# Performance work log

Hardware: AMD Instinct MI355X
Metric: run time of the kernel (lower is better)

Reference implementation:

```python
import jax, jax.numpy as jnp
import numpy as np

H = 256          # decoder_size
MAX_LENGTH = 64
VOCAB = 3


def _cell(x, h, c, w_ih, w_hh, b_ih, b_hh):
    # PyTorch LSTM cell, gate order i, f, g, o
    g = x @ w_ih.T + h @ w_hh.T + b_ih + b_hh
    i, f, gg, o = jnp.split(g, 4, axis=-1)
    c = jax.nn.sigmoid(f) * c + jax.nn.sigmoid(i) * jnp.tanh(gg)
    h = jax.nn.sigmoid(o) * jnp.tanh(c)
    return h, c


def _final_state(xs, w_ih, w_hh, b_ih, b_hh):
    # run a unidirectional LSTM over xs [T,B,D], return final (h, c)
    B = xs.shape[1]
    h0 = jnp.zeros((B, H), xs.dtype)
    c0 = jnp.zeros((B, H), xs.dtype)
    def step(carry, x):
        h, c = _cell(x, carry[0], carry[1], w_ih, w_hh, b_ih, b_hh)
        return (h, c), None
    (h, c), _ = jax.lax.scan(step, (h0, c0), xs)
    return h, c


def setup_inputs() -> dict:
    key = jax.random.key(0)
    ks = jax.random.split(key, 20)
    T, B, D = 512, 128, 1024
    s = jnp.float32(0.05)  # keep gates out of saturation
    def p(k, shape):
        return jax.random.normal(k, shape, jnp.float32) * s
    return {
        "x": jax.random.normal(ks[0], (T, B, D), jnp.float32),
        "ew_ih_f": p(ks[1], (4 * H, D)), "ew_hh_f": p(ks[2], (4 * H, H)),
        "eb_ih_f": p(ks[3], (4 * H,)),   "eb_hh_f": p(ks[4], (4 * H,)),
        "ew_ih_b": p(ks[5], (4 * H, D)), "ew_hh_b": p(ks[6], (4 * H, H)),
        "eb_ih_b": p(ks[7], (4 * H,)),   "eb_hh_b": p(ks[8], (4 * H,)),
        "dw_ih0": p(ks[9], (4 * H, H)),  "dw_hh0": p(ks[10], (4 * H, H)),
        "db_ih0": p(ks[11], (4 * H,)),   "db_hh0": p(ks[12], (4 * H,)),
        "dw_ih1": p(ks[13], (4 * H, H)), "dw_hh1": p(ks[14], (4 * H, H)),
        "db_ih1": p(ks[15], (4 * H,)),   "db_hh1": p(ks[16], (4 * H,)),
        "lw": p(ks[17], (VOCAB, H)),     "lb": p(ks[18], (VOCAB,)),
    }


def reference(x, ew_ih_f, ew_hh_f, eb_ih_f, eb_hh_f,
              ew_ih_b, ew_hh_b, eb_ih_b, eb_hh_b,
              dw_ih0, dw_hh0, db_ih0, db_hh0,
              dw_ih1, dw_hh1, db_ih1, db_hh1,
              lw, lb):
    # --- bidirectional encoder: only final hidden states are used ---
    hf, cf = _final_state(x, ew_ih_f, ew_hh_f, eb_ih_f, eb_hh_f)          # forward dir
    hb, cb = _final_state(x[::-1], ew_ih_b, ew_hh_b, eb_ih_b, eb_hh_b)    # backward dir
    # encoder h_n/c_n stacked as [fwd, bwd] -> decoder layer0, layer1 init
    B = x.shape[1]
    inp0 = jnp.zeros((B, H), x.dtype)
    def step(carry, _):
        inp, h0, c0, h1, c1 = carry
        h0, c0 = _cell(inp, h0, c0, dw_ih0, dw_hh0, db_ih0, db_hh0)
        h1, c1 = _cell(h0, h1, c1, dw_ih1, dw_hh1, db_ih1, db_hh1)
        out = h1 @ lw.T + lb  # [B, VOCAB]
        return (h1, h0, c0, h1, c1), out
    _, outs = jax.lax.scan(step, (inp0, hf, cf, hb, cb), None, length=MAX_LENGTH)
    return outs  # [MAX_LENGTH, B, VOCAB]
```

## Files before the change

kernel.cpp:

```cpp
#include <hip/hip_runtime.h>
#include <hip/hip_bf16.h>
#include <math.h>


typedef unsigned short u16;
typedef unsigned int u32;
typedef unsigned long long u64;
typedef _Float16 f16;
typedef f16 f16x8 __attribute__((ext_vector_type(8)));
typedef u16 u16x8 __attribute__((ext_vector_type(8)));
typedef u32 u32x4 __attribute__((ext_vector_type(4)));
typedef float f32x4 __attribute__((ext_vector_type(4)));

__device__ __forceinline__ u16 f2h(float f) {
  return __builtin_bit_cast(unsigned short, (f16)f);
}
__device__ __forceinline__ float h2f(u16 h) {
  return (float)__builtin_bit_cast(f16, h);
}
__device__ __forceinline__ u32 packf16(float a, float b) {
  return (u32)f2h(a) | ((u32)f2h(b) << 16);
}
__device__ __forceinline__ u64 ald64(const u64* p) {
  return __hip_atomic_load(p, __ATOMIC_RELAXED, __HIP_MEMORY_SCOPE_AGENT);
}
__device__ __forceinline__ void ast64(u64* p, u64 v) {
  __hip_atomic_store(p, v, __ATOMIC_RELAXED, __HIP_MEMORY_SCOPE_AGENT);
}

#define SENT 0xFFFFFFFFFFFFFFFFull

__global__ __launch_bounds__(256) void init_k(u32* hglob, u32* r0, u32* r1) {
  int gid = blockIdx.x * 256 + threadIdx.x;
  if (gid < 131072)       hglob[gid] = 0xFFFFFFFFu;
  else if (gid < 196608)  r0[gid - 131072] = 0xFFFFFFFFu;
  else                    r1[gid - 196608] = 0xFFFFFFFFu;
}

__global__ __launch_bounds__(256) void convert_k(
    const float* __restrict__ x,
    const float* __restrict__ wfm, const float* __restrict__ wbm,
    const float* __restrict__ bif, const float* __restrict__ bhf,
    const float* __restrict__ bib, const float* __restrict__ bhb,
    const float* __restrict__ dbi0, const float* __restrict__ dbh0,
    const float* __restrict__ dbi1, const float* __restrict__ dbh1,
    u16* __restrict__ xh, u16* __restrict__ wh,
    float* __restrict__ bias2, float* __restrict__ dbias) {
  const long NX = 67108864L, NW = 1048576L;
  long gid = (long)blockIdx.x * 256 + threadIdx.x;
  if (gid < 1024) {
    bias2[gid]        = bif[gid] + bhf[gid];
    bias2[1024 + gid] = bib[gid] + bhb[gid];
    dbias[gid]        = dbi0[gid] + dbh0[gid];
    dbias[1024 + gid] = dbi1[gid] + dbh1[gid];
  }
  long total4 = (NX + 2 * NW) >> 2;
  long stride = (long)gridDim.x * 256;
  for (long q = gid; q < total4; q += stride) {
    long i = q << 2;
    const float* src; u16* dst; long o;
    if (i < NX)            { src = x;   dst = xh;      o = i; }
    else if (i < NX + NW)  { src = wfm; dst = wh;      o = i - NX; }
    else                   { src = wbm; dst = wh + NW; o = i - NX - NW; }
    float4 v = *(const float4*)&src[o];
    dst[o + 0] = f2h(v.x); dst[o + 1] = f2h(v.y);
    dst[o + 2] = f2h(v.z); dst[o + 3] = f2h(v.w);
  }
}

__global__ __launch_bounds__(256) void convert_we3_k(
    const float* __restrict__ whf, const float* __restrict__ whb,
    u16* __restrict__ wenc3) {
  int o = blockIdx.x * 256 + threadIdx.x;
  int j = o & 7, lane = (o >> 3) & 63, ks = (o >> 9) & 7;
  int w = (o >> 12) & 3, cg = (o >> 14) & 15, d = o >> 18;
  int ri = lane & 15;
  int gcol = (ri & 3) * 256 + cg * 16 + w * 4 + (ri >> 2);
  int k = ks * 32 + (lane >> 4) * 8 + j;
  const float* wsrc = d ? whb : whf;
  wenc3[o] = f2h(wsrc[gcol * 256 + k]);
}

__global__ __launch_bounds__(256) void convert_wdec_k(
    const float* __restrict__ wi0, const float* __restrict__ wh0,
    const float* __restrict__ wi1, const float* __restrict__ wh1,
    u16* __restrict__ wdec) {
  int o = blockIdx.x * 256 + threadIdx.x;
  int j = o & 7, lane = (o >> 3) & 63, ks = (o >> 9) & 15;
  int w = (o >> 13) & 3, cg = (o >> 15) & 15, L = o >> 19;
  int ri = lane & 15;
  int row = (ri & 3) * 256 + cg * 16 + w * 4 + (ri >> 2);
  int k = ks * 32 + (lane >> 4) * 8 + j;
  const float* wi = L ? wi1 : wi0;
  const float* wh = L ? wh1 : wh0;
  float v = (k < 256) ? wi[row * 256 + k] : wh[row * 256 + k - 256];
  wdec[o] = f2h(v);
}

__global__ __launch_bounds__(256) void xproj_gemm(
    const u16* __restrict__ xh, const u16* __restrict__ wh,
    const float* __restrict__ bias2, float* __restrict__ xp) {
  __shared__ u16 Al[128][40];
  __shared__ u16 Bl[128][40];
  int bid = blockIdx.x;
  int dir = bid >> 12, rem = bid & 4095, tb = rem >> 3, nb = rem & 7;
  int tsrc = dir ? (511 - tb) : tb;
  const u16* A  = xh + (long)tsrc * (128 * 1024);
  const u16* Bw = wh + (long)dir * (1024 * 1024) + (long)nb * (128 * 1024);
  float* C = xp + ((long)(dir * 512 + tb) * 128) * 1024 + nb * 128;
  const float* bias = bias2 + dir * 1024 + nb * 128;

  int tid = threadIdx.x, lane = tid & 63, wid = tid >> 6;
  int wr = wid >> 1, wc = wid & 1;
  int srow = tid >> 1, scol = (tid & 1) * 16;
  int fr = lane & 15, ko = lane >> 4;

  f32x4 acc[4][4] = {};
  for (int k0 = 0; k0 < 1024; k0 += 32) {
    u16x8 a0 = *(const u16x8*)&A[(long)srow * 1024 + k0 + scol];
    u16x8 a1 = *(const u16x8*)&A[(long)srow * 1024 + k0 + scol + 8];
    u16x8 b0 = *(const u16x8*)&Bw[(long)srow * 1024 + k0 + scol];
    u16x8 b1 = *(const u16x8*)&Bw[(long)srow * 1024 + k0 + scol + 8];
    __syncthreads();
    *(u16x8*)&Al[srow][scol]     = a0;
    *(u16x8*)&Al[srow][scol + 8] = a1;
    *(u16x8*)&Bl[srow][scol]     = b0;
    *(u16x8*)&Bl[srow][scol + 8] = b1;
    __syncthreads();
    f16x8 af[4], bf[4];
#pragma unroll
    for (int i = 0; i < 4; ++i)
      af[i] = __builtin_bit_cast(f16x8, *(const u16x8*)&Al[wr * 64 + i * 16 + fr][ko * 8]);
#pragma unroll
    for (int jf = 0; jf < 4; ++jf)
      bf[jf] = __builtin_bit_cast(f16x8, *(const u16x8*)&Bl[wc * 64 + jf * 16 + fr][ko * 8]);
#pragma unroll
    for (int i = 0; i < 4; ++i)
#pragma unroll
      for (int jf = 0; jf < 4; ++jf)
        acc[i][jf] = __builtin_amdgcn_mfma_f32_16x16x32_f16(af[i], bf[jf], acc[i][jf], 0, 0, 0);
  }
  int fq = lane >> 4;
#pragma unroll
  for (int i = 0; i < 4; ++i)
#pragma unroll
    for (int jf = 0; jf < 4; ++jf) {
      int col = wc * 64 + jf * 16 + fr;
      float bv = bias[col];
#pragma unroll
      for (int e = 0; e < 4; ++e) {
        int row = wr * 64 + i * 16 + fq * 4 + e;
        C[(long)row * 1024 + col] = acc[i][jf][e] + bv;
      }
    }
}

__global__ __launch_bounds__(256, 1) void encoder_k(
    const u16* __restrict__ wenc3, const float* __restrict__ xp,
    u32* hglob,
    float* h0b, float* h1b, float* cfb, float* cbb) {
  int b = blockIdx.x;
  int g16 = ((b >> 7) << 3) | (b & 7);
  int cg = (b >> 3) & 15;
  int d = g16 >> 3, bg = g16 & 7;
  int tid = threadIdx.x, lane = tid & 63, w = tid >> 6;
  int brow = lane & 15, lq = lane >> 4;
  int hswz = (brow & 7) << 4;

  __shared__ __align__(16) char hlds[2][8192];
  __shared__ __align__(16) u16 hstage[16][16];

  f16x8 wfr[8];
  {
    const u16* wb = wenc3 + (((long)d * 16 + cg) * 4 + w) * 4096 + lane * 8;
#pragma unroll
    for (int ks = 0; ks < 8; ++ks)
      wfr[ks] = __builtin_bit_cast(f16x8, *(const u16x8*)(wb + (long)ks * 512));
  }

  float c_state = 0.f;
  long xpbase = ((long)(d * 512) * 128 + bg * 16 + brow) * 1024 + cg * 16 + w * 4 + lq;
  float xpv[4], xpn[4];
#pragma unroll
  for (int g = 0; g < 4; ++g) xpv[g] = xp[xpbase + g * 256];

  u64* hg = (u64*)hglob;
  long ringbase = (long)g16 * 4096;
  int gcg = tid >> 4, gbrow = tid & 15;
  int gldsbase = gbrow * 512 + gcg * 32;
  int gswz = (gbrow & 7) << 4;
  __syncthreads();

  for (int t = 0; t < 512; ++t) {
    if (t != 0) {
      const long gb = ringbase + (long)(t & 3) * 1024 + 4 * tid;
      u64 v0 = SENT, v1 = SENT, v2 = SENT, v3 = SENT;
      for (;;) {
        bool ok = true;
        if (v0 == SENT) { v0 = ald64(hg + gb + 0); ok &= (v0 != SENT); }
        if (v1 == SENT) { v1 = ald64(hg + gb + 1); ok &= (v1 != SENT); }
        if (v2 == SENT) { v2 = ald64(hg + gb + 2); ok &= (v2 != SENT); }
        if (v3 == SENT) { v3 = ald64(hg + gb + 3); ok &= (v3 != SENT); }
        if (ok) break;
      }
      if (tid < 64)
        ast64(hg + ringbase + (long)((t + 2) & 3) * 1024 + cg * 64 + tid, SENT);
#pragma unroll
      for (int g = 0; g < 4; ++g) xpv[g] = xpn[g];
      char* hwr = hlds[t & 1];
      *(u32x4*)(hwr + (gldsbase ^ gswz)) =
          (u32x4){ (u32)v0, (u32)(v0 >> 32), (u32)v1, (u32)(v1 >> 32) };
      *(u32x4*)(hwr + ((gldsbase + 16) ^ gswz)) =
          (u32x4){ (u32)v2, (u32)(v2 >> 32), (u32)v3, (u32)(v3 >> 32) };
    }
    if (t < 511) {
      long xb2 = xpbase + (long)(t + 1) * 131072;
#pragma unroll
      for (int g = 0; g < 4; ++g) xpn[g] = xp[xb2 + g * 256];
    }
    __syncthreads();

    f32x4 acc0 = {}, acc1 = {};
    if (t != 0) {
      const char* hrd = hlds[t & 1];
#pragma unroll
      for (int ks = 0; ks < 8; ++ks) {
        f16x8 hf = *(const f16x8*)(hrd + ((brow * 512 + ks * 64 + lq * 16) ^ hswz));
        if (ks & 1) acc1 = __builtin_amdgcn_mfma_f32_16x16x32_f16(wfr[ks], hf, acc1, 0, 0, 0);
        else        acc0 = __builtin_amdgcn_mfma_f32_16x16x32_f16(wfr[ks], hf, acc0, 0, 0, 0);
      }
    }

    float iv = 1.f / (1.f + expf(-(acc0[0] + acc1[0] + xpv[0])));
    float fv = 1.f / (1.f + expf(-(acc0[1] + acc1[1] + xpv[1])));
    float gg = tanhf(acc0[2] + acc1[2] + xpv[2]);
    float ov = 1.f / (1.f + expf(-(acc0[3] + acc1[3] + xpv[3])));
    c_state = fv * c_state + iv * gg;
    float hval = ov * tanhf(c_state);

    if (t < 511) {
      hstage[brow][w * 4 + lq] = f2h(hval);
      __syncthreads();
      asm volatile("s_waitcnt vmcnt(0)" ::: "memory");
      if (tid < 64) {
        u64 v = *(const u64*)&hstage[tid >> 2][(tid & 3) * 4];
        ast64(hg + ringbase + (long)((t + 1) & 3) * 1024 + cg * 64 + tid, v);
      }
    } else {
      int rowg = bg * 16 + brow, colg = cg * 16 + w * 4 + lq;
      (d ? h1b : h0b)[32768 + rowg * 256 + colg] = hval;
      (d ? cbb : cfb)[rowg * 256 + colg] = c_state;
    }
  }
}

__global__ __launch_bounds__(256, 1) void decoder_k(
    const u16* __restrict__ wdec, const float* __restrict__ dbias,
    const float* __restrict__ h0b, const float* __restrict__ h1b,
    const float* __restrict__ cfb, const float* __restrict__ cbb,
    u32* r0, u32* r1, float* __restrict__ hist) {
  int b = blockIdx.x;
  int bg = b & 7, cg = b >> 3;
  int tid = threadIdx.x, lane = tid & 63, w = tid >> 6;
  int brow = lane & 15, lq = lane >> 4;
  int hswz = (brow & 7) << 4;
  int col = cg * 16 + w * 4 + lq;

  __shared__ __align__(16) char hA[8192];
  __shared__ __align__(16) char hB[8192];
  __shared__ __align__(16) u16 hstage[16][16];

  f16x8 w0[16], w1[16];
  {
    const u16* p0 = wdec + ((long)(cg * 4 + w)) * 8192 + lane * 8;
    const u16* p1 = wdec + ((long)((16 + cg) * 4 + w)) * 8192 + lane * 8;
#pragma unroll
    for (int ks = 0; ks < 16; ++ks) {
      w0[ks] = __builtin_bit_cast(f16x8, *(const u16x8*)(p0 + (long)ks * 512));
      w1[ks] = __builtin_bit_cast(f16x8, *(const u16x8*)(p1 + (long)ks * 512));
    }
  }
  float b0[4], b1[4];
#pragma unroll
  for (int g = 0; g < 4; ++g) {
    b0[g] = dbias[g * 256 + col];
    b1[g] = dbias[1024 + g * 256 + col];
  }
  float c0 = cfb[(bg * 16 + brow) * 256 + col];
  float c1 = cbb[(bg * 16 + brow) * 256 + col];

  int gbrow = tid & 15, gcg = tid >> 4;
  int gldsbase = gbrow * 512 + gcg * 32;
  int gswz = (gbrow & 7) << 4;
  {
    const float* sA = h0b + 32768 + (bg * 16 + gbrow) * 256 + gcg * 16;
    const float* sB = h1b + 32768 + (bg * 16 + gbrow) * 256 + gcg * 16;
    u32 wa[8], wb[8];
#pragma unroll
    for (int i = 0; i < 8; ++i) {
      wa[i] = packf16(sA[2 * i], sA[2 * i + 1]);
      wb[i] = packf16(sB[2 * i], sB[2 * i + 1]);
    }
    *(u32x4*)(hA + (gldsbase ^ gswz))        = (u32x4){wa[0], wa[1], wa[2], wa[3]};
    *(u32x4*)(hA + ((gldsbase + 16) ^ gswz)) = (u32x4){wa[4], wa[5], wa[6], wa[7]};
    *(u32x4*)(hB + (gldsbase ^ gswz))        = (u32x4){wb[0], wb[1], wb[2], wb[3]};
    *(u32x4*)(hB + ((gldsbase + 16) ^ gswz)) = (u32x4){wb[4], wb[5], wb[6], wb[7]};
  }
  __syncthreads();

  u64* g0 = (u64*)r0;
  u64* g1 = (u64*)r1;
  long ring = (long)bg * 4096;

  for (int t = 0; t < 64; ++t) {
    f32x4 a0 = {}, a1 = {};
    if (t > 0) {
#pragma unroll
      for (int ks = 0; ks < 8; ++ks) {
        f16x8 hf = *(const f16x8*)(hB + ((brow * 512 + ks * 64 + lq * 16) ^ hswz));
        if (ks & 1) a1 = __builtin_amdgcn_mfma_f32_16x16x32_f16(w0[ks], hf, a1, 0, 0, 0);
        else        a0 = __builtin_amdgcn_mfma_f32_16x16x32_f16(w0[ks], hf, a0, 0, 0, 0);
      }
    }
#pragma unroll
    for (int ks = 0; ks < 8; ++ks) {
      f16x8 hf = *(const f16x8*)(hA + ((brow * 512 + ks * 64 + lq * 16) ^ hswz));
      if (ks & 1) a1 = __builtin_amdgcn_mfma_f32_16x16x32_f16(w0[8 + ks], hf, a1, 0, 0, 0);
      else        a0 = __builtin_amdgcn_mfma_f32_16x16x32_f16(w0[8 + ks], hf, a0, 0, 0, 0);
    }
    {
      float iv = 1.f / (1.f + expf(-(a0[0] + a1[0] + b0[0])));
      float fv = 1.f / (1.f + expf(-(a0[1] + a1[1] + b0[1])));
      float gg = tanhf(a0[2] + a1[2] + b0[2]);
      float ov = 1.f / (1.f + expf(-(a0[3] + a1[3] + b0[3])));
      c0 = fv * c0 + iv * gg;
      float h0v = ov * tanhf(c0);
      hstage[brow][w * 4 + lq] = f2h(h0v);
    }
    __syncthreads();
    if (tid < 64)
      ast64(g0 + ring + (long)((t + 2) & 3) * 1024 + cg * 64 + tid, SENT);
    asm volatile("s_waitcnt vmcnt(0)" ::: "memory");
    if (tid < 64) {
      u64 v = *(const u64*)&hstage[tid >> 2][(tid & 3) * 4];
      ast64(g0 + ring + (long)(t & 3) * 1024 + cg * 64 + tid, v);
    }
    {
      const long gb = ring + (long)(t & 3) * 1024 + 4 * tid;
      u64 v0 = SENT, v1 = SENT, v2 = SENT, v3 = SENT;
      for (;;) {
        bool ok = true;
        if (v0 == SENT) { v0 = ald64(g0 + gb + 0); ok &= (v0 != SENT); }
        if (v1 == SENT) { v1 = ald64(g0 + gb + 1); ok &= (v1 != SENT); }
        if (v2 == SENT) { v2 = ald64(g0 + gb + 2); ok &= (v2 != SENT); }
        if (v3 == SENT) { v3 = ald64(g0 + gb + 3); ok &= (v3 != SENT); }
        if (ok) break;
      }
      *(u32x4*)(hA + (gldsbase ^ gswz)) =
          (u32x4){ (u32)v0, (u32)(v0 >> 32), (u32)v1, (u32)(v1 >> 32) };
      *(u32x4*)(hA + ((gldsbase + 16) ^ gswz)) =
          (u32x4){ (u32)v2, (u32)(v2 >> 32), (u32)v3, (u32)(v3 >> 32) };
    }
    __syncthreads();

    a0 = (f32x4){}; a1 = (f32x4){};
#pragma unroll
    for (int ks = 0; ks < 8; ++ks) {
      f16x8 hf = *(const f16x8*)(hA + ((brow * 512 + ks * 64 + lq * 16) ^ hswz));
      if (ks & 1) a1 = __builtin_amdgcn_mfma_f32_16x16x32_f16(w1[ks], hf, a1, 0, 0, 0);
      else        a0 = __builtin_amdgcn_mfma_f32_16x16x32_f16(w1[ks], hf, a0, 0, 0, 0);
    }
#pragma unroll
    for (int ks = 0; ks < 8; ++ks) {
      f16x8 hf = *(const f16x8*)(hB + ((brow * 512 + ks * 64 + lq * 16) ^ hswz));
      if (ks & 1) a1 = __builtin_amdgcn_mfma_f32_16x16x32_f16(w1[8 + ks], hf, a1, 0, 0, 0);
      else        a0 = __builtin_amdgcn_mfma_f32_16x16x32_f16(w1[8 + ks], hf, a0, 0, 0, 0);
    }
    {
      float iv = 1.f / (1.f + expf(-(a0[0] + a1[0] + b1[0])));
      float fv = 1.f / (1.f + expf(-(a0[1] + a1[1] + b1[1])));
      float gg = tanhf(a0[2] + a1[2] + b1[2]);
      float ov = 1.f / (1.f + expf(-(a0[3] + a1[3] + b1[3])));
      c1 = fv * c1 + iv * gg;
      float h1v = ov * tanhf(c1);
      hstage[brow][w * 4 + lq] = f2h(h1v);
    }
    __syncthreads();
    if (tid < 64) {
      u64 v = *(const u64*)&hstage[tid >> 2][(tid & 3) * 4];
      float4 hv4 = { h2f((u16)v), h2f((u16)(v >> 16)),
                     h2f((u16)(v >> 32)), h2f((u16)(v >> 48)) };
      *(float4*)&hist[((long)t * 128 + bg * 16 + (tid >> 2)) * 256 + cg * 16 + (tid & 3) * 4] = hv4;
    }
    if (t < 63) {
      if (tid < 64)
        ast64(g1 + ring + (long)((t + 2) & 3) * 1024 + cg * 64 + tid, SENT);
      asm volatile("s_waitcnt vmcnt(0)" ::: "memory");
      if (tid < 64) {
        u64 v = *(const u64*)&hstage[tid >> 2][(tid & 3) * 4];
        ast64(g1 + ring + (long)(t & 3) * 1024 + cg * 64 + tid, v);
      }
      const long gb = ring + (long)(t & 3) * 1024 + 4 * tid;
      u64 v0 = SENT, v1 = SENT, v2 = SENT, v3 = SENT;
      for (;;) {
        bool ok = true;
        if (v0 == SENT) { v0 = ald64(g1 + gb + 0); ok &= (v0 != SENT); }
        if (v1 == SENT) { v1 = ald64(g1 + gb + 1); ok &= (v1 != SENT); }
        if (v2 == SENT) { v2 = ald64(g1 + gb + 2); ok &= (v2 != SENT); }
        if (v3 == SENT) { v3 = ald64(g1 + gb + 3); ok &= (v3 != SENT); }
        if (ok) break;
      }
      *(u32x4*)(hB + (gldsbase ^ gswz)) =
          (u32x4){ (u32)v0, (u32)(v0 >> 32), (u32)v1, (u32)(v1 >> 32) };
      *(u32x4*)(hB + ((gldsbase + 16) ^ gswz)) =
          (u32x4){ (u32)v2, (u32)(v2 >> 32), (u32)v3, (u32)(v3 >> 32) };
    }
    __syncthreads();
  }
}

__global__ __launch_bounds__(256) void logits_k(
    const float* __restrict__ hist, const float* __restrict__ lw,
    const float* __restrict__ lb, float* __restrict__ out) {
  int widx = threadIdx.x >> 6, lane = threadIdx.x & 63;
  int row = blockIdx.x * 4 + widx;
  const float* h = hist + (long)row * 256;
  float4 hv = *(const float4*)&h[lane * 4];
  float s[3];
#pragma unroll
  for (int v = 0; v < 3; ++v) {
    float4 wv = *(const float4*)&lw[v * 256 + lane * 4];
    float p = hv.x * wv.x + hv.y * wv.y + hv.z * wv.z + hv.w * wv.w;
#pragma unroll
    for (int o = 32; o > 0; o >>= 1) p += __shfl_xor(p, o, 64);
    s[v] = p;
  }
  if (lane == 0) {
    out[row * 3 + 0] = s[0] + lb[0];
    out[row * 3 + 1] = s[1] + lb[1];
    out[row * 3 + 2] = s[2] + lb[2];
  }
}

extern "C" void kernel_launch(void* const* d_in, const int* in_sizes, int n_in,
                              void* d_out, int out_size, void* d_ws, size_t ws_size,
                              hipStream_t stream) {
  const float* x     = (const float*)d_in[0];
  const float* ewihf = (const float*)d_in[1];
  const float* ewhhf = (const float*)d_in[2];
  const float* ebihf = (const float*)d_in[3];
  const float* ebhhf = (const float*)d_in[4];
  const float* ewihb = (const float*)d_in[5];
  const float* ewhhb = (const float*)d_in[6];
  const float* ebihb = (const float*)d_in[7];
  const float* ebhhb = (const float*)d_in[8];
  const float* dwih0 = (const float*)d_in[9];
  const float* dwhh0 = (const float*)d_in[10];
  const float* dbih0 = (const float*)d_in[11];
  const float* dbhh0 = (const float*)d_in[12];
  const float* dwih1 = (const float*)d_in[13];
  const float* dwhh1 = (const float*)d_in[14];
  const float* dbih1 = (const float*)d_in[15];
  const float* dbhh1 = (const float*)d_in[16];
  const float* lw    = (const float*)d_in[17];
  const float* lb    = (const float*)d_in[18];
  float* out = (float*)d_out;
  (void)in_sizes; (void)n_in; (void)out_size; (void)ws_size;

  char* wsb = (char*)d_ws;
  size_t off = 0;
  auto take = [&](size_t bytes) -> char* {
    char* p = wsb + off;
    off = (off + bytes + 255) & ~(size_t)255;
    return p;
  };
  u16*   xh    = (u16*)take(67108864ull * 2);
  u16*   whx   = (u16*)take(2097152ull * 2);
  float* xp    = (float*)take(134217728ull * 4);
  u16*   wenc3 = (u16*)take(524288ull * 2);
  u16*   wdec  = (u16*)take(1048576ull * 2);
  float* bias2 = (float*)take(2048 * 4);
  float* dbias = (float*)take(2048 * 4);
  u32*   hglob = (u32*)take(131072ull * 4);
  u32*   r0    = (u32*)take(65536ull * 4);
  u32*   r1    = (u32*)take(65536ull * 4);
  float* h0b   = (float*)take(65536 * 4);
  float* h1b   = (float*)take(65536 * 4);
  float* cfb   = (float*)take(32768 * 4);
  float* cbb   = (float*)take(32768 * 4);
  float* hist  = (float*)take(2097152 * 4);

  init_k<<<1024, 256, 0, stream>>>(hglob, r0, r1);
  convert_k<<<2048, 256, 0, stream>>>(x, ewihf, ewihb, ebihf, ebhhf, ebihb, ebhhb,
                                      dbih0, dbhh0, dbih1, dbhh1, xh, whx, bias2, dbias);
  convert_we3_k<<<2048, 256, 0, stream>>>(ewhhf, ewhhb, wenc3);
  convert_wdec_k<<<4096, 256, 0, stream>>>(dwih0, dwhh0, dwih1, dwhh1, wdec);
  xproj_gemm<<<8192, 256, 0, stream>>>(xh, whx, bias2, xp);
  encoder_k<<<256, 256, 0, stream>>>(wenc3, xp, hglob, h0b, h1b, cfb, cbb);
  decoder_k<<<128, 256, 0, stream>>>(wdec, dbias, h0b, h1b, cfb, cbb, r0, r1, hist);
  logits_k<<<2048, 256, 0, stream>>>(hist, lw, lb, out);
}
```

Before: 2.226 ms.

## Repartition encoder recurrence into paired 512-thread blocks with half-hidden ownership

The encoder recurrence moves from 256 blocks (each owning 16 hidden columns and exchanging h through a global ring with all 16 column-group peers) to 32 blocks of 512 threads. Each block owns half the hidden columns for one direction and batch group, keeps 4 weight tiles in registers, and swaps only the other half with a single partner block every step. The aim is to cut cross-block polling and synchronisation latency on the serial 512-step chain. In exchange each block does four times the MFMA and gate work per step, uses far fewer CUs, and raises register pressure.

```diff
diff --git a/kernel.cpp b/kernel.cpp
--- a/kernel.cpp
+++ b/kernel.cpp
@@ -68,17 +68,17 @@
   }
 }
 
-__global__ __launch_bounds__(256) void convert_we3_k(
+__global__ __launch_bounds__(256) void convert_we4_k(
     const float* __restrict__ whf, const float* __restrict__ whb,
-    u16* __restrict__ wenc3) {
+    u16* __restrict__ wenc4) {
   int o = blockIdx.x * 256 + threadIdx.x;
   int j = o & 7, lane = (o >> 3) & 63, ks = (o >> 9) & 7;
-  int w = (o >> 12) & 3, cg = (o >> 14) & 15, d = o >> 18;
+  int tile = (o >> 12) & 3, w = (o >> 14) & 7, half = (o >> 17) & 1, d = o >> 18;
   int ri = lane & 15;
-  int gcol = (ri & 3) * 256 + cg * 16 + w * 4 + (ri >> 2);
+  int gcol = (ri & 3) * 256 + half * 128 + w * 16 + tile * 4 + (ri >> 2);
   int k = ks * 32 + (lane >> 4) * 8 + j;
   const float* wsrc = d ? whb : whf;
-  wenc3[o] = f2h(wsrc[gcol * 256 + k]);
+  wenc4[o] = f2h(wsrc[gcol * 256 + k]);
 }
 
 __global__ __launch_bounds__(256) void convert_wdec_k(
@@ -155,101 +155,101 @@
     }
 }
 
-__global__ __launch_bounds__(256, 1) void encoder_k(
-    const u16* __restrict__ wenc3, const float* __restrict__ xp,
+__global__ __launch_bounds__(512, 2) void encoder_k(
+    const u16* __restrict__ wenc4, const float* __restrict__ xp,
     u32* hglob,
     float* h0b, float* h1b, float* cfb, float* cbb) {
   int b = blockIdx.x;
-  int g16 = ((b >> 7) << 3) | (b & 7);
-  int cg = (b >> 3) & 15;
-  int d = g16 >> 3, bg = g16 & 7;
+  int d = b >> 4, bg = (b >> 1) & 7, half = b & 1;
   int tid = threadIdx.x, lane = tid & 63, w = tid >> 6;
   int brow = lane & 15, lq = lane >> 4;
   int hswz = (brow & 7) << 4;
+  int ohb = half * 256;
+  int phb = (half ^ 1) * 256;
 
   __shared__ __align__(16) char hlds[2][8192];
-  __shared__ __align__(16) u16 hstage[16][16];
-
-  f16x8 wfr[8];
-  {
-    const u16* wb = wenc3 + (((long)d * 16 + cg) * 4 + w) * 4096 + lane * 8;
+  __shared__ __align__(16) u16 hstage[16][128];
+
+  f16x8 wfr[32];
+#pragma unroll
+  for (int tile = 0; tile < 4; ++tile) {
+    const u16* wb = wenc4 + ((((long)(d * 2 + half) * 8 + w) * 4 + tile)) * 4096 + lane * 8;
 #pragma unroll
     for (int ks = 0; ks < 8; ++ks)
-      wfr[ks] = __builtin_bit_cast(f16x8, *(const u16x8*)(wb + (long)ks * 512));
-  }
-
-  float c_state = 0.f;
-  long xpbase = ((long)(d * 512) * 128 + bg * 16 + brow) * 1024 + cg * 16 + w * 4 + lq;
-  float xpv[4], xpn[4];
-#pragma unroll
-  for (int g = 0; g < 4; ++g) xpv[g] = xp[xpbase + g * 256];
+      wfr[tile * 8 + ks] = __builtin_bit_cast(f16x8, *(const u16x8*)(wb + (long)ks * 512));
+  }
+
+  float c_state[4];
+#pragma unroll
+  for (int i = 0; i < 4; ++i) c_state[i] = 0.f;
+
+  long xprow = ((long)(d * 512) * 128 + bg * 16 + brow) * 1024;
+  int xcol0 = half * 128 + w * 16 + lq;
+  float xpv[4][4];
+#pragma unroll
+  for (int tile = 0; tile < 4; ++tile)
+#pragma unroll
+    for (int g = 0; g < 4; ++g)
+      xpv[tile][g] = xp[xprow + g * 256 + xcol0 + tile * 4];
 
   u64* hg = (u64*)hglob;
-  long ringbase = (long)g16 * 4096;
-  int gcg = tid >> 4, gbrow = tid & 15;
-  int gldsbase = gbrow * 512 + gcg * 32;
-  int gswz = (gbrow & 7) << 4;
+  long orbase = (long)(((d * 8 + bg) * 2) + half) * 2048;
+  long prbase = (long)(((d * 8 + bg) * 2) + (half ^ 1)) * 2048;
+  int srow2 = tid >> 5, scolq = tid & 31;
   __syncthreads();
 
   for (int t = 0; t < 512; ++t) {
     if (t != 0) {
-      const long gb = ringbase + (long)(t & 3) * 1024 + 4 * tid;
-      u64 v0 = SENT, v1 = SENT, v2 = SENT, v3 = SENT;
-      for (;;) {
-        bool ok = true;
-        if (v0 == SENT) { v0 = ald64(hg + gb + 0); ok &= (v0 != SENT); }
-        if (v1 == SENT) { v1 = ald64(hg + gb + 1); ok &= (v1 != SENT); }
-        if (v2 == SENT) { v2 = ald64(hg + gb + 2); ok &= (v2 != SENT); }
-        if (v3 == SENT) { v3 = ald64(hg + gb + 3); ok &= (v3 != SENT); }
-        if (ok) break;
-      }
-      if (tid < 64)
-        ast64(hg + ringbase + (long)((t + 2) & 3) * 1024 + cg * 64 + tid, SENT);
-#pragma unroll
-      for (int g = 0; g < 4; ++g) xpv[g] = xpn[g];
-      char* hwr = hlds[t & 1];
-      *(u32x4*)(hwr + (gldsbase ^ gswz)) =
-          (u32x4){ (u32)v0, (u32)(v0 >> 32), (u32)v1, (u32)(v1 >> 32) };
-      *(u32x4*)(hwr + ((gldsbase + 16) ^ gswz)) =
-          (u32x4){ (u32)v2, (u32)(v2 >> 32), (u32)v3, (u32)(v3 >> 32) };
-    }
-    if (t < 511) {
-      long xb2 = xpbase + (long)(t + 1) * 131072;
-#pragma unroll
-      for (int g = 0; g < 4; ++g) xpn[g] = xp[xb2 + g * 256];
-    }
-    __syncthreads();
-
-    f32x4 acc0 = {}, acc1 = {};
+      const u64* pp = hg + prbase + (long)(t & 3) * 512 + tid;
+      u64 v = ald64(pp);
+      while (v == SENT) v = ald64(pp);
+      ast64(hg + orbase + (long)((t + 2) & 3) * 512 + tid, SENT);
+      *(u64*)(hlds[t & 1] + ((srow2 * 512 + phb + scolq * 8) ^ ((srow2 & 7) << 4))) = v;
+    }
+    __syncthreads();
+
+    f32x4 acc[4] = {};
     if (t != 0) {
       const char* hrd = hlds[t & 1];
 #pragma unroll
       for (int ks = 0; ks < 8; ++ks) {
         f16x8 hf = *(const f16x8*)(hrd + ((brow * 512 + ks * 64 + lq * 16) ^ hswz));
-        if (ks & 1) acc1 = __builtin_amdgcn_mfma_f32_16x16x32_f16(wfr[ks], hf, acc1, 0, 0, 0);
-        else        acc0 = __builtin_amdgcn_mfma_f32_16x16x32_f16(wfr[ks], hf, acc0, 0, 0, 0);
-      }
-    }
-
-    float iv = 1.f / (1.f + expf(-(acc0[0] + acc1[0] + xpv[0])));
-    float fv = 1.f / (1.f + expf(-(acc0[1] + acc1[1] + xpv[1])));
-    float gg = tanhf(acc0[2] + acc1[2] + xpv[2]);
-    float ov = 1.f / (1.f + expf(-(acc0[3] + acc1[3] + xpv[3])));
-    c_state = fv * c_state + iv * gg;
-    float hval = ov * tanhf(c_state);
+#pragma unroll
+        for (int tile = 0; tile < 4; ++tile)
+          acc[tile] = __builtin_amdgcn_mfma_f32_16x16x32_f16(wfr[tile * 8 + ks], hf, acc[tile], 0, 0, 0);
+      }
+    }
+
+#pragma unroll
+    for (int tile = 0; tile < 4; ++tile) {
+      float iv = 1.f / (1.f + expf(-(acc[tile][0] + xpv[tile][0])));
+      float fv = 1.f / (1.f + expf(-(acc[tile][1] + xpv[tile][1])));
+      float gg = tanhf(acc[tile][2] + xpv[tile][2]);
+      float ov = 1.f / (1.f + expf(-(acc[tile][3] + xpv[tile][3])));
+      float c2 = fv * c_state[tile] + iv * gg;
+      c_state[tile] = c2;
+      float hval = ov * tanhf(c2);
+      if (t < 511) {
+        hstage[brow][w * 16 + tile * 4 + lq] = f2h(hval);
+      } else {
+        int rowg = bg * 16 + brow, colg = half * 128 + w * 16 + tile * 4 + lq;
+        (d ? h1b : h0b)[32768 + rowg * 256 + colg] = hval;
+        (d ? cbb : cfb)[rowg * 256 + colg] = c_state[tile];
+      }
+    }
 
     if (t < 511) {
-      hstage[brow][w * 4 + lq] = f2h(hval);
       __syncthreads();
       asm volatile("s_waitcnt vmcnt(0)" ::: "memory");
-      if (tid < 64) {
-        u64 v = *(const u64*)&hstage[tid >> 2][(tid & 3) * 4];
-        ast64(hg + ringbase + (long)((t + 1) & 3) * 1024 + cg * 64 + tid, v);
-      }
-    } else {
-      int rowg = bg * 16 + brow, colg = cg * 16 + w * 4 + lq;
-      (d ? h1b : h0b)[32768 + rowg * 256 + colg] = hval;
-      (d ? cbb : cfb)[rowg * 256 + colg] = c_state;
+      u64 sv = *(const u64*)&hstage[srow2][scolq * 4];
+      ast64(hg + orbase + (long)((t + 1) & 3) * 512 + tid, sv);
+      *(u64*)(hlds[(t + 1) & 1] + ((srow2 * 512 + ohb + scolq * 8) ^ ((srow2 & 7) << 4))) = sv;
+      long xb2 = xprow + (long)(t + 1) * 131072;
+#pragma unroll
+      for (int tile = 0; tile < 4; ++tile)
+#pragma unroll
+        for (int g = 0; g < 4; ++g)
+          xpv[tile][g] = xp[xb2 + g * 256 + xcol0 + tile * 4];
     }
   }
 }
@@ -477,7 +477,7 @@
   u16*   xh    = (u16*)take(67108864ull * 2);
   u16*   whx   = (u16*)take(2097152ull * 2);
   float* xp    = (float*)take(134217728ull * 4);
-  u16*   wenc3 = (u16*)take(524288ull * 2);
+  u16*   wenc4 = (u16*)take(524288ull * 2);
   u16*   wdec  = (u16*)take(1048576ull * 2);
   float* bias2 = (float*)take(2048 * 4);
   float* dbias = (float*)take(2048 * 4);
@@ -493,10 +493,10 @@
   init_k<<<1024, 256, 0, stream>>>(hglob, r0, r1);
   convert_k<<<2048, 256, 0, stream>>>(x, ewihf, ewihb, ebihf, ebhhf, ebihb, ebhhb,
                                       dbih0, dbhh0, dbih1, dbhh1, xh, whx, bias2, dbias);
-  convert_we3_k<<<2048, 256, 0, stream>>>(ewhhf, ewhhb, wenc3);
+  convert_we4_k<<<2048, 256, 0, stream>>>(ewhhf, ewhhb, wenc4);
   convert_wdec_k<<<4096, 256, 0, stream>>>(dwih0, dwhh0, dwih1, dwhh1, wdec);
   xproj_gemm<<<8192, 256, 0, stream>>>(xh, whx, bias2, xp);
-  encoder_k<<<256, 256, 0, stream>>>(wenc3, xp, hglob, h0b, h1b, cfb, cbb);
+  encoder_k<<<32, 512, 0, stream>>>(wenc4, xp, hglob, h0b, h1b, cfb, cbb);
   decoder_k<<<128, 256, 0, stream>>>(wdec, dbias, h0b, h1b, cfb, cbb, r0, r1, hist);
   logits_k<<<2048, 256, 0, stream>>>(hist, lw, lb, out);
 }
```

New measurement: 4.346 ms. 95.2% more time.
